# Kernel optimization log

Hardware: AMD Instinct MI355X
Metric: run time of the kernel (lower is better)

## Reference

```python
import jax, jax.numpy as jnp
import numpy as np

DIM = 768
HID = 4 * DIM
NUM_EXPERTS = 8


def setup_inputs() -> dict:
    key = jax.random.key(0)
    ks = jax.random.split(key, 8)
    B, T = 2, 2048
    x = jax.random.normal(ks[0], (B, T, DIM), dtype=jnp.float32)
    mapped_tokens = jax.random.randint(ks[1], (B * T,), 0, NUM_EXPERTS)
    s_in = 1.0 / np.sqrt(DIM)   # nn.Linear init scale for fan_in=DIM
    s_hid = 1.0 / np.sqrt(HID)  # for fan_in=HID
    Wg = jax.random.uniform(ks[2], (NUM_EXPERTS, DIM, HID), jnp.float32, -s_in, s_in)
    bg = jax.random.uniform(ks[3], (NUM_EXPERTS, HID), jnp.float32, -s_in, s_in)
    Wi = jax.random.uniform(ks[4], (NUM_EXPERTS, DIM, HID), jnp.float32, -s_in, s_in)
    bi = jax.random.uniform(ks[5], (NUM_EXPERTS, HID), jnp.float32, -s_in, s_in)
    Wo = jax.random.uniform(ks[6], (NUM_EXPERTS, HID, DIM), jnp.float32, -s_hid, s_hid)
    bo = jax.random.uniform(ks[7], (NUM_EXPERTS, DIM), jnp.float32, -s_hid, s_hid)
    return {"x": x, "mapped_tokens": mapped_tokens, "Wg": Wg, "bg": bg,
            "Wi": Wi, "bi": bi, "Wo": Wo, "bo": bo}


def reference(x, mapped_tokens, Wg, bg, Wi, bi, Wo, bo):
    B, T, C = x.shape
    xf = x.reshape(-1, C)                      # [N, C], N = B*T
    out = jnp.zeros_like(xf)
    E = Wg.shape[0]
    for e in range(E):                         # small fixed expert loop
        h = jax.nn.silu(xf @ Wg[e] + bg[e]) * (xf @ Wi[e] + bi[e])  # [N, 4C]
        y = h @ Wo[e] + bo[e]                  # [N, C]
        out = out + jnp.where((mapped_tokens == e)[:, None], y, 0.0)
    return out.reshape(B, T, C)
```

## Files before the change

kernel.cpp:

```cpp
#include <hip/hip_runtime.h>
#include <hip/hip_bf16.h>
#include <stdint.h>

#define DIM 768
#define HID 3072
#define NE 8
#define NTOK 4096
#define PADROWS 5120
#define MAXT 40

#define M_PO 0
#define M_NTILES 24
#define M_TE 25
#define M_TR 65
#define M_TV 105
#define M_PERM 256
#define XE_OFF (64 * 1024)
#define H_OFF  8126464

typedef short short8 __attribute__((ext_vector_type(8)));
typedef short short4v __attribute__((ext_vector_type(4)));
typedef float f32x4 __attribute__((ext_vector_type(4)));

__device__ __forceinline__ short f2bf(float f) {
  union { float f; uint32_t u; } in; in.f = f;
  uint32_t u = in.u;
  uint32_t r = (u + 0x7fffu + ((u >> 16) & 1u)) >> 16;
  return (short)r;
}

__global__ void route_kernel(const int* __restrict__ map, int* __restrict__ meta) {
  __shared__ int scnt[NE];
  __shared__ int scur[NE];
  int t = threadIdx.x;
  if (t < NE) scnt[t] = 0;
  __syncthreads();
  for (int i = t; i < NTOK; i += 256) atomicAdd(&scnt[map[i]], 1);
  __syncthreads();
  if (t == 0) {
    int acc = 0, nt = 0;
    for (int e = 0; e < NE; ++e) {
      meta[M_PO + e] = acc;
      scur[e] = acc;
      int c = scnt[e];
      for (int r = 0; r < c; r += 128) {
        meta[M_TE + nt] = e;
        meta[M_TR + nt] = acc + r;
        meta[M_TV + nt] = (c - r < 128) ? (c - r) : 128;
        ++nt;
      }
      acc += (c + 127) & ~127;
    }
    meta[M_PO + 8] = acc;
    meta[M_NTILES] = nt;
  }
  for (int i = t; i < PADROWS; i += 256) meta[M_PERM + i] = 0;
  __syncthreads();
  for (int i = t; i < NTOK; i += 256) {
    int e = map[i];
    int slot = atomicAdd(&scur[e], 1);
    meta[M_PERM + slot] = i;
  }
}

__global__ void gather_kernel(const float* __restrict__ x, const int* __restrict__ meta,
                              short* __restrict__ Xe) {
  int id = blockIdx.x * 256 + threadIdx.x;
  if (id >= PADROWS * 96) return;
  int row = id / 96;
  int sub = id - row * 96;
  int tok = meta[M_PERM + row];
  const float* src = x + (size_t)tok * DIM + sub * 8;
  float4 a = *(const float4*)src;
  float4 b = *(const float4*)(src + 4);
  short8 v;
  v[0] = f2bf(a.x); v[1] = f2bf(a.y); v[2] = f2bf(a.z); v[3] = f2bf(a.w);
  v[4] = f2bf(b.x); v[5] = f2bf(b.y); v[6] = f2bf(b.z); v[7] = f2bf(b.w);
  int blk = sub >> 3, s = sub & 7;
  int off = row * (DIM * 2) + blk * 128 + ((s * 16) ^ ((row & 7) << 4));
  *(short8*)((char*)Xe + off) = v;
}

__launch_bounds__(256)
__global__ void gemm1_kernel(const short* __restrict__ Xe, const float* __restrict__ Wg,
                             const float* __restrict__ bg, const float* __restrict__ Wi,
                             const float* __restrict__ bi, const int* __restrict__ meta,
                             short* __restrict__ H) {
  int nt = meta[M_NTILES];
  int ty = blockIdx.y;
  if (ty >= nt) return;
  int e = meta[M_TE + ty], row0 = meta[M_TR + ty], rows = meta[M_TV + ty];
  int j0 = blockIdx.x * 64;
  __shared__ short As[128 * 64];
  __shared__ short Bt[2][64 * 64];
  int tid = threadIdx.x;
  int lane = tid & 63, w = tid >> 6;
  int wm = w >> 1, wn = w & 1;
  const float* W0 = Wg + (size_t)e * DIM * HID;
  const float* W1 = Wi + (size_t)e * DIM * HID;
  f32x4 ag[4][2] = {};
  f32x4 av[4][2] = {};
  int kb = tid >> 4, jb = tid & 15;
  for (int kt = 0; kt < DIM / 64; ++kt) {
    __syncthreads();
    #pragma unroll
    for (int q = 0; q < 4; ++q) {
      int rr = (w * 4 + q) * 8 + (lane >> 3);
      const char* src = (const char*)Xe + (size_t)(row0 + rr) * (DIM * 2) + kt * 128 + (lane & 7) * 16;
      __builtin_amdgcn_global_load_lds((const __attribute__((address_space(1))) void*)src,
                                       (__attribute__((address_space(3))) void*)((char*)As + (w * 4 + q) * 1024),
                                       16, 0, 0);
    }
    #pragma unroll
    for (int mat = 0; mat < 2; ++mat) {
      const float* Wp = (mat == 0) ? W0 : W1;
      const float* base = Wp + (size_t)(kt * 64 + kb * 4) * HID + j0 + jb * 4;
      float4 r0 = *(const float4*)(base);
      float4 r1 = *(const float4*)(base + HID);
      float4 r2 = *(const float4*)(base + 2 * HID);
      float4 r3 = *(const float4*)(base + 3 * HID);
      char* bt = (char*)&Bt[mat][0];
      int col = jb * 4;
      {
        short4v s; s[0]=f2bf(r0.x); s[1]=f2bf(r1.x); s[2]=f2bf(r2.x); s[3]=f2bf(r3.x);
        int c2 = col + 0; *(short4v*)(bt + c2 * 128 + ((kb * 8) ^ ((c2 & 7) << 4))) = s;
      }
      {
        short4v s; s[0]=f2bf(r0.y); s[1]=f2bf(r1.y); s[2]=f2bf(r2.y); s[3]=f2bf(r3.y);
        int c2 = col + 1; *(short4v*)(bt + c2 * 128 + ((kb * 8) ^ ((c2 & 7) << 4))) = s;
      }
      {
        short4v s; s[0]=f2bf(r0.z); s[1]=f2bf(r1.z); s[2]=f2bf(r2.z); s[3]=f2bf(r3.z);
        int c2 = col + 2; *(short4v*)(bt + c2 * 128 + ((kb * 8) ^ ((c2 & 7) << 4))) = s;
      }
      {
        short4v s; s[0]=f2bf(r0.w); s[1]=f2bf(r1.w); s[2]=f2bf(r2.w); s[3]=f2bf(r3.w);
        int c2 = col + 3; *(short4v*)(bt + c2 * 128 + ((kb * 8) ^ ((c2 & 7) << 4))) = s;
      }
    }
    __syncthreads();
    #pragma unroll
    for (int kf = 0; kf < 2; ++kf) {
      short8 af[4];
      #pragma unroll
      for (int m = 0; m < 4; ++m) {
        int r = wm * 64 + m * 16 + (lane & 15);
        int coff = (kf * 64 + (lane >> 4) * 16) ^ ((r & 7) << 4);
        af[m] = *(const short8*)((const char*)As + r * 128 + coff);
      }
      #pragma unroll
      for (int n = 0; n < 2; ++n) {
        int c = wn * 32 + n * 16 + (lane & 15);
        int coff = (kf * 64 + (lane >> 4) * 16) ^ ((c & 7) << 4);
        short8 b0 = *(const short8*)((const char*)&Bt[0][0] + c * 128 + coff);
        short8 b1 = *(const short8*)((const char*)&Bt[1][0] + c * 128 + coff);
        #pragma unroll
        for (int m = 0; m < 4; ++m) {
          ag[m][n] = __builtin_amdgcn_mfma_f32_16x16x32_bf16(af[m], b0, ag[m][n], 0, 0, 0);
          av[m][n] = __builtin_amdgcn_mfma_f32_16x16x32_bf16(af[m], b1, av[m][n], 0, 0, 0);
        }
      }
    }
  }
  #pragma unroll
  for (int n = 0; n < 2; ++n) {
    int c = j0 + wn * 32 + n * 16 + (lane & 15);
    float bgv = bg[e * HID + c];
    float biv = bi[e * HID + c];
    #pragma unroll
    for (int m = 0; m < 4; ++m) {
      #pragma unroll
      for (int r = 0; r < 4; ++r) {
        int rl = wm * 64 + m * 16 + (lane >> 4) * 4 + r;
        if (rl < rows) {
          float g = ag[m][n][r] + bgv;
          float v = av[m][n][r] + biv;
          float h = g / (1.f + __expf(-g)) * v;
          int grow = row0 + rl;
          int off = grow * (HID * 2) + (c >> 6) * 128 + ((2 * (c & 63)) ^ ((grow & 7) << 4));
          *(short*)((char*)H + off) = f2bf(h);
        }
      }
    }
  }
}

__launch_bounds__(256)
__global__ void gemm2_kernel(const short* __restrict__ H, const float* __restrict__ Wo,
                             const float* __restrict__ bo, const int* __restrict__ meta,
                             float* __restrict__ out) {
  int nt = meta[M_NTILES];
  int ty = blockIdx.y;
  if (ty >= nt) return;
  int e = meta[M_TE + ty], row0 = meta[M_TR + ty], rows = meta[M_TV + ty];
  int j0 = blockIdx.x * 64;
  __shared__ short As[128 * 64];
  __shared__ short Bt[64 * 64];
  int tid = threadIdx.x;
  int lane = tid & 63, w = tid >> 6;
  int wm = w >> 1, wn = w & 1;
  const float* W2 = Wo + (size_t)e * HID * DIM;
  f32x4 acc[4][2] = {};
  int kb = tid >> 4, jb = tid & 15;
  for (int kt = 0; kt < HID / 64; ++kt) {
    __syncthreads();
    #pragma unroll
    for (int q = 0; q < 4; ++q) {
      int rr = (w * 4 + q) * 8 + (lane >> 3);
      const char* src = (const char*)H + (size_t)(row0 + rr) * (HID * 2) + kt * 128 + (lane & 7) * 16;
      __builtin_amdgcn_global_load_lds((const __attribute__((address_space(1))) void*)src,
                                       (__attribute__((address_space(3))) void*)((char*)As + (w * 4 + q) * 1024),
                                       16, 0, 0);
    }
    {
      const float* base = W2 + (size_t)(kt * 64 + kb * 4) * DIM + j0 + jb * 4;
      float4 r0 = *(const float4*)(base);
      float4 r1 = *(const float4*)(base + DIM);
      float4 r2 = *(const float4*)(base + 2 * DIM);
      float4 r3 = *(const float4*)(base + 3 * DIM);
      char* bt = (char*)&Bt[0];
      int col = jb * 4;
      {
        short4v s; s[0]=f2bf(r0.x); s[1]=f2bf(r1.x); s[2]=f2bf(r2.x); s[3]=f2bf(r3.x);
        int c2 = col + 0; *(short4v*)(bt + c2 * 128 + ((kb * 8) ^ ((c2 & 7) << 4))) = s;
      }
      {
        short4v s; s[0]=f2bf(r0.y); s[1]=f2bf(r1.y); s[2]=f2bf(r2.y); s[3]=f2bf(r3.y);
        int c2 = col + 1; *(short4v*)(bt + c2 * 128 + ((kb * 8) ^ ((c2 & 7) << 4))) = s;
      }
      {
        short4v s; s[0]=f2bf(r0.z); s[1]=f2bf(r1.z); s[2]=f2bf(r2.z); s[3]=f2bf(r3.z);
        int c2 = col + 2; *(short4v*)(bt + c2 * 128 + ((kb * 8) ^ ((c2 & 7) << 4))) = s;
      }
      {
        short4v s; s[0]=f2bf(r0.w); s[1]=f2bf(r1.w); s[2]=f2bf(r2.w); s[3]=f2bf(r3.w);
        int c2 = col + 3; *(short4v*)(bt + c2 * 128 + ((kb * 8) ^ ((c2 & 7) << 4))) = s;
      }
    }
    __syncthreads();
    #pragma unroll
    for (int kf = 0; kf < 2; ++kf) {
      short8 af[4];
      #pragma unroll
      for (int m = 0; m < 4; ++m) {
        int r = wm * 64 + m * 16 + (lane & 15);
        int coff = (kf * 64 + (lane >> 4) * 16) ^ ((r & 7) << 4);
        af[m] = *(const short8*)((const char*)As + r * 128 + coff);
      }
      #pragma unroll
      for (int n = 0; n < 2; ++n) {
        int c = wn * 32 + n * 16 + (lane & 15);
        int coff = (kf * 64 + (lane >> 4) * 16) ^ ((c & 7) << 4);
        short8 b0 = *(const short8*)((const char*)&Bt[0] + c * 128 + coff);
        #pragma unroll
        for (int m = 0; m < 4; ++m) {
          acc[m][n] = __builtin_amdgcn_mfma_f32_16x16x32_bf16(af[m], b0, acc[m][n], 0, 0, 0);
        }
      }
    }
  }
  #pragma unroll
  for (int n = 0; n < 2; ++n) {
    int c = j0 + wn * 32 + n * 16 + (lane & 15);
    float bov = bo[e * DIM + c];
    #pragma unroll
    for (int m = 0; m < 4; ++m) {
      #pragma unroll
      for (int r = 0; r < 4; ++r) {
        int rl = wm * 64 + m * 16 + (lane >> 4) * 4 + r;
        if (rl < rows) {
          int tok = meta[M_PERM + row0 + rl];
          out[(size_t)tok * DIM + c] = acc[m][n][r] + bov;
        }
      }
    }
  }
}

extern "C" void kernel_launch(void* const* d_in, const int* in_sizes, int n_in,
                              void* d_out, int out_size, void* d_ws, size_t ws_size,
                              hipStream_t stream) {
  (void)in_sizes; (void)n_in; (void)out_size; (void)ws_size;
  const float* x   = (const float*)d_in[0];
  const int*   map = (const int*)d_in[1];
  const float* Wg  = (const float*)d_in[2];
  const float* bg  = (const float*)d_in[3];
  const float* Wi  = (const float*)d_in[4];
  const float* bi  = (const float*)d_in[5];
  const float* Wo  = (const float*)d_in[6];
  const float* bo  = (const float*)d_in[7];
  float* out = (float*)d_out;
  int* meta = (int*)d_ws;
  short* Xe = (short*)((char*)d_ws + XE_OFF);
  short* H  = (short*)((char*)d_ws + H_OFF);

  hipLaunchKernelGGL(route_kernel, dim3(1), dim3(256), 0, stream, map, meta);
  hipLaunchKernelGGL(gather_kernel, dim3(PADROWS * 96 / 256), dim3(256), 0, stream, x, meta, Xe);
  hipLaunchKernelGGL(gemm1_kernel, dim3(HID / 64, MAXT), dim3(256), 0, stream,
                     Xe, Wg, bg, Wi, bi, meta, H);
  hipLaunchKernelGGL(gemm2_kernel, dim3(DIM / 64, MAXT), dim3(256), 0, stream,
                     H, Wo, bo, meta, out);
}
```

Measured before the change: 412.0 us.

## Software-pipeline both expert GEMMs with double-buffered A tiles and register-prefetched weights

Both GEMM kernels now prefetch the next K-tile: activations go asynchronously into a second LDS buffer, and fp32 weights are loaded into registers while the current tile's MFMAs run. The bf16 weight tile is written to LDS after a barrier, so global latency overlaps with compute instead of stalling each iteration. The thread-to-(kb,jb) mapping is swapped, bf16 conversion uses the library intrinsic, and launch bounds request 3 blocks per CU. The costs are more registers and double the A-tile LDS, and the single-buffered B tile still needs two barriers per iteration.

```diff
diff --git a/kernel.cpp b/kernel.cpp
--- a/kernel.cpp
+++ b/kernel.cpp
@@ -22,11 +22,9 @@
 typedef short short4v __attribute__((ext_vector_type(4)));
 typedef float f32x4 __attribute__((ext_vector_type(4)));
 
-__device__ __forceinline__ short f2bf(float f) {
-  union { float f; uint32_t u; } in; in.f = f;
-  uint32_t u = in.u;
-  uint32_t r = (u + 0x7fffu + ((u >> 16) & 1u)) >> 16;
-  return (short)r;
+__device__ __forceinline__ short bfs(float f) {
+  __hip_bfloat16 h = __float2bfloat16(f);
+  short s; __builtin_memcpy(&s, &h, 2); return s;
 }
 
 __global__ void route_kernel(const int* __restrict__ map, int* __restrict__ meta) {
@@ -74,14 +72,45 @@
   float4 a = *(const float4*)src;
   float4 b = *(const float4*)(src + 4);
   short8 v;
-  v[0] = f2bf(a.x); v[1] = f2bf(a.y); v[2] = f2bf(a.z); v[3] = f2bf(a.w);
-  v[4] = f2bf(b.x); v[5] = f2bf(b.y); v[6] = f2bf(b.z); v[7] = f2bf(b.w);
+  v[0] = bfs(a.x); v[1] = bfs(a.y); v[2] = bfs(a.z); v[3] = bfs(a.w);
+  v[4] = bfs(b.x); v[5] = bfs(b.y); v[6] = bfs(b.z); v[7] = bfs(b.w);
   int blk = sub >> 3, s = sub & 7;
   int off = row * (DIM * 2) + blk * 128 + ((s * 16) ^ ((row & 7) << 4));
   *(short8*)((char*)Xe + off) = v;
 }
 
-__launch_bounds__(256)
+__device__ __forceinline__ void write_bt2(char* bt0, char* bt1,
+                                          const float4 (&br)[2][4], int kb, int jb) {
+  char* bts[2] = {bt0, bt1};
+  #pragma unroll
+  for (int mat = 0; mat < 2; ++mat) {
+    #pragma unroll
+    for (int i = 0; i < 4; ++i) {
+      int c2 = jb * 4 + i;
+      short4v s;
+      s[0] = bfs(((const float*)&br[mat][0])[i]);
+      s[1] = bfs(((const float*)&br[mat][1])[i]);
+      s[2] = bfs(((const float*)&br[mat][2])[i]);
+      s[3] = bfs(((const float*)&br[mat][3])[i]);
+      *(short4v*)(bts[mat] + c2 * 128 + ((kb * 8) ^ ((c2 & 7) << 4))) = s;
+    }
+  }
+}
+
+__device__ __forceinline__ void write_bt1(char* bt, const float4 (&br)[4], int kb, int jb) {
+  #pragma unroll
+  for (int i = 0; i < 4; ++i) {
+    int c2 = jb * 4 + i;
+    short4v s;
+    s[0] = bfs(((const float*)&br[0])[i]);
+    s[1] = bfs(((const float*)&br[1])[i]);
+    s[2] = bfs(((const float*)&br[2])[i]);
+    s[3] = bfs(((const float*)&br[3])[i]);
+    *(short4v*)(bt + c2 * 128 + ((kb * 8) ^ ((c2 & 7) << 4))) = s;
+  }
+}
+
+__launch_bounds__(256, 3)
 __global__ void gemm1_kernel(const short* __restrict__ Xe, const float* __restrict__ Wg,
                              const float* __restrict__ bg, const float* __restrict__ Wi,
                              const float* __restrict__ bi, const int* __restrict__ meta,
@@ -91,54 +120,53 @@
   if (ty >= nt) return;
   int e = meta[M_TE + ty], row0 = meta[M_TR + ty], rows = meta[M_TV + ty];
   int j0 = blockIdx.x * 64;
-  __shared__ short As[128 * 64];
+  __shared__ short As[2][128 * 64];
   __shared__ short Bt[2][64 * 64];
   int tid = threadIdx.x;
   int lane = tid & 63, w = tid >> 6;
   int wm = w >> 1, wn = w & 1;
+  int kb = tid & 15, jb = tid >> 4;
   const float* W0 = Wg + (size_t)e * DIM * HID;
   const float* W1 = Wi + (size_t)e * DIM * HID;
   f32x4 ag[4][2] = {};
   f32x4 av[4][2] = {};
-  int kb = tid >> 4, jb = tid & 15;
-  for (int kt = 0; kt < DIM / 64; ++kt) {
-    __syncthreads();
-    #pragma unroll
-    for (int q = 0; q < 4; ++q) {
-      int rr = (w * 4 + q) * 8 + (lane >> 3);
-      const char* src = (const char*)Xe + (size_t)(row0 + rr) * (DIM * 2) + kt * 128 + (lane & 7) * 16;
-      __builtin_amdgcn_global_load_lds((const __attribute__((address_space(1))) void*)src,
-                                       (__attribute__((address_space(3))) void*)((char*)As + (w * 4 + q) * 1024),
-                                       16, 0, 0);
-    }
-    #pragma unroll
-    for (int mat = 0; mat < 2; ++mat) {
-      const float* Wp = (mat == 0) ? W0 : W1;
-      const float* base = Wp + (size_t)(kt * 64 + kb * 4) * HID + j0 + jb * 4;
-      float4 r0 = *(const float4*)(base);
-      float4 r1 = *(const float4*)(base + HID);
-      float4 r2 = *(const float4*)(base + 2 * HID);
-      float4 r3 = *(const float4*)(base + 3 * HID);
-      char* bt = (char*)&Bt[mat][0];
-      int col = jb * 4;
-      {
-        short4v s; s[0]=f2bf(r0.x); s[1]=f2bf(r1.x); s[2]=f2bf(r2.x); s[3]=f2bf(r3.x);
-        int c2 = col + 0; *(short4v*)(bt + c2 * 128 + ((kb * 8) ^ ((c2 & 7) << 4))) = s;
-      }
-      {
-        short4v s; s[0]=f2bf(r0.y); s[1]=f2bf(r1.y); s[2]=f2bf(r2.y); s[3]=f2bf(r3.y);
-        int c2 = col + 1; *(short4v*)(bt + c2 * 128 + ((kb * 8) ^ ((c2 & 7) << 4))) = s;
-      }
-      {
-        short4v s; s[0]=f2bf(r0.z); s[1]=f2bf(r1.z); s[2]=f2bf(r2.z); s[3]=f2bf(r3.z);
-        int c2 = col + 2; *(short4v*)(bt + c2 * 128 + ((kb * 8) ^ ((c2 & 7) << 4))) = s;
-      }
-      {
-        short4v s; s[0]=f2bf(r0.w); s[1]=f2bf(r1.w); s[2]=f2bf(r2.w); s[3]=f2bf(r3.w);
-        int c2 = col + 3; *(short4v*)(bt + c2 * 128 + ((kb * 8) ^ ((c2 & 7) << 4))) = s;
-      }
-    }
-    __syncthreads();
+  float4 br[2][4];
+
+  #pragma unroll
+  for (int mat = 0; mat < 2; ++mat) {
+    const float* base = (mat ? W1 : W0) + (size_t)(kb * 4) * HID + j0 + jb * 4;
+    #pragma unroll
+    for (int r = 0; r < 4; ++r) br[mat][r] = *(const float4*)(base + r * HID);
+  }
+  #pragma unroll
+  for (int q = 0; q < 4; ++q) {
+    const char* src = (const char*)Xe + (size_t)(row0 + (w * 4 + q) * 8 + (lane >> 3)) * (DIM * 2)
+                      + (lane & 7) * 16;
+    __builtin_amdgcn_global_load_lds((const __attribute__((address_space(1))) void*)src,
+                                     (__attribute__((address_space(3))) void*)((char*)&As[0][0] + (w * 4 + q) * 1024),
+                                     16, 0, 0);
+  }
+  write_bt2((char*)&Bt[0][0], (char*)&Bt[1][0], br, kb, jb);
+  __syncthreads();
+
+  int cur = 0;
+  for (int kt = 0; kt < 12; ++kt) {
+    if (kt < 11) {
+      #pragma unroll
+      for (int mat = 0; mat < 2; ++mat) {
+        const float* base = (mat ? W1 : W0) + (size_t)((kt + 1) * 64 + kb * 4) * HID + j0 + jb * 4;
+        #pragma unroll
+        for (int r = 0; r < 4; ++r) br[mat][r] = *(const float4*)(base + r * HID);
+      }
+      #pragma unroll
+      for (int q = 0; q < 4; ++q) {
+        const char* src = (const char*)Xe + (size_t)(row0 + (w * 4 + q) * 8 + (lane >> 3)) * (DIM * 2)
+                          + (kt + 1) * 128 + (lane & 7) * 16;
+        __builtin_amdgcn_global_load_lds((const __attribute__((address_space(1))) void*)src,
+                                         (__attribute__((address_space(3))) void*)((char*)&As[cur ^ 1][0] + (w * 4 + q) * 1024),
+                                         16, 0, 0);
+      }
+    }
     #pragma unroll
     for (int kf = 0; kf < 2; ++kf) {
       short8 af[4];
@@ -146,7 +174,7 @@
       for (int m = 0; m < 4; ++m) {
         int r = wm * 64 + m * 16 + (lane & 15);
         int coff = (kf * 64 + (lane >> 4) * 16) ^ ((r & 7) << 4);
-        af[m] = *(const short8*)((const char*)As + r * 128 + coff);
+        af[m] = *(const short8*)((const char*)&As[cur][0] + r * 128 + coff);
       }
       #pragma unroll
       for (int n = 0; n < 2; ++n) {
@@ -161,7 +189,12 @@
         }
       }
     }
-  }
+    asm volatile("s_waitcnt lgkmcnt(0)\n\ts_barrier" ::: "memory");
+    if (kt < 11) write_bt2((char*)&Bt[0][0], (char*)&Bt[1][0], br, kb, jb);
+    __syncthreads();
+    cur ^= 1;
+  }
+
   #pragma unroll
   for (int n = 0; n < 2; ++n) {
     int c = j0 + wn * 32 + n * 16 + (lane & 15);
@@ -178,14 +211,14 @@
           float h = g / (1.f + __expf(-g)) * v;
           int grow = row0 + rl;
           int off = grow * (HID * 2) + (c >> 6) * 128 + ((2 * (c & 63)) ^ ((grow & 7) << 4));
-          *(short*)((char*)H + off) = f2bf(h);
+          *(short*)((char*)H + off) = bfs(h);
         }
       }
     }
   }
 }
 
-__launch_bounds__(256)
+__launch_bounds__(256, 3)
 __global__ void gemm2_kernel(const short* __restrict__ H, const float* __restrict__ Wo,
                              const float* __restrict__ bo, const int* __restrict__ meta,
                              float* __restrict__ out) {
@@ -194,50 +227,45 @@
   if (ty >= nt) return;
   int e = meta[M_TE + ty], row0 = meta[M_TR + ty], rows = meta[M_TV + ty];
   int j0 = blockIdx.x * 64;
-  __shared__ short As[128 * 64];
+  __shared__ short As[2][128 * 64];
   __shared__ short Bt[64 * 64];
   int tid = threadIdx.x;
   int lane = tid & 63, w = tid >> 6;
   int wm = w >> 1, wn = w & 1;
+  int kb = tid & 15, jb = tid >> 4;
   const float* W2 = Wo + (size_t)e * HID * DIM;
   f32x4 acc[4][2] = {};
-  int kb = tid >> 4, jb = tid & 15;
-  for (int kt = 0; kt < HID / 64; ++kt) {
-    __syncthreads();
-    #pragma unroll
-    for (int q = 0; q < 4; ++q) {
-      int rr = (w * 4 + q) * 8 + (lane >> 3);
-      const char* src = (const char*)H + (size_t)(row0 + rr) * (HID * 2) + kt * 128 + (lane & 7) * 16;
-      __builtin_amdgcn_global_load_lds((const __attribute__((address_space(1))) void*)src,
-                                       (__attribute__((address_space(3))) void*)((char*)As + (w * 4 + q) * 1024),
-                                       16, 0, 0);
-    }
-    {
-      const float* base = W2 + (size_t)(kt * 64 + kb * 4) * DIM + j0 + jb * 4;
-      float4 r0 = *(const float4*)(base);
-      float4 r1 = *(const float4*)(base + DIM);
-      float4 r2 = *(const float4*)(base + 2 * DIM);
-      float4 r3 = *(const float4*)(base + 3 * DIM);
-      char* bt = (char*)&Bt[0];
-      int col = jb * 4;
-      {
-        short4v s; s[0]=f2bf(r0.x); s[1]=f2bf(r1.x); s[2]=f2bf(r2.x); s[3]=f2bf(r3.x);
-        int c2 = col + 0; *(short4v*)(bt + c2 * 128 + ((kb * 8) ^ ((c2 & 7) << 4))) = s;
-      }
-      {
-        short4v s; s[0]=f2bf(r0.y); s[1]=f2bf(r1.y); s[2]=f2bf(r2.y); s[3]=f2bf(r3.y);
-        int c2 = col + 1; *(short4v*)(bt + c2 * 128 + ((kb * 8) ^ ((c2 & 7) << 4))) = s;
-      }
-      {
-        short4v s; s[0]=f2bf(r0.z); s[1]=f2bf(r1.z); s[2]=f2bf(r2.z); s[3]=f2bf(r3.z);
-        int c2 = col + 2; *(short4v*)(bt + c2 * 128 + ((kb * 8) ^ ((c2 & 7) << 4))) = s;
-      }
-      {
-        short4v s; s[0]=f2bf(r0.w); s[1]=f2bf(r1.w); s[2]=f2bf(r2.w); s[3]=f2bf(r3.w);
-        int c2 = col + 3; *(short4v*)(bt + c2 * 128 + ((kb * 8) ^ ((c2 & 7) << 4))) = s;
-      }
-    }
-    __syncthreads();
+  float4 br[4];
+
+  #pragma unroll
+  for (int r = 0; r < 4; ++r)
+    br[r] = *(const float4*)(W2 + (size_t)(kb * 4 + r) * DIM + j0 + jb * 4);
+  #pragma unroll
+  for (int q = 0; q < 4; ++q) {
+    const char* src = (const char*)H + (size_t)(row0 + (w * 4 + q) * 8 + (lane >> 3)) * (HID * 2)
+                      + (lane & 7) * 16;
+    __builtin_amdgcn_global_load_lds((const __attribute__((address_space(1))) void*)src,
+                                     (__attribute__((address_space(3))) void*)((char*)&As[0][0] + (w * 4 + q) * 1024),
+                                     16, 0, 0);
+  }
+  write_bt1((char*)&Bt[0], br, kb, jb);
+  __syncthreads();
+
+  int cur = 0;
+  for (int kt = 0; kt < 48; ++kt) {
+    if (kt < 47) {
+      #pragma unroll
+      for (int r = 0; r < 4; ++r)
+        br[r] = *(const float4*)(W2 + (size_t)((kt + 1) * 64 + kb * 4 + r) * DIM + j0 + jb * 4);
+      #pragma unroll
+      for (int q = 0; q < 4; ++q) {
+        const char* src = (const char*)H + (size_t)(row0 + (w * 4 + q) * 8 + (lane >> 3)) * (HID * 2)
+                          + (kt + 1) * 128 + (lane & 7) * 16;
+        __builtin_amdgcn_global_load_lds((const __attribute__((address_space(1))) void*)src,
+                                         (__attribute__((address_space(3))) void*)((char*)&As[cur ^ 1][0] + (w * 4 + q) * 1024),
+                                         16, 0, 0);
+      }
+    }
     #pragma unroll
     for (int kf = 0; kf < 2; ++kf) {
       short8 af[4];
@@ -245,7 +273,7 @@
       for (int m = 0; m < 4; ++m) {
         int r = wm * 64 + m * 16 + (lane & 15);
         int coff = (kf * 64 + (lane >> 4) * 16) ^ ((r & 7) << 4);
-        af[m] = *(const short8*)((const char*)As + r * 128 + coff);
+        af[m] = *(const short8*)((const char*)&As[cur][0] + r * 128 + coff);
       }
       #pragma unroll
       for (int n = 0; n < 2; ++n) {
@@ -258,7 +286,12 @@
         }
       }
     }
-  }
+    asm volatile("s_waitcnt lgkmcnt(0)\n\ts_barrier" ::: "memory");
+    if (kt < 47) write_bt1((char*)&Bt[0], br, kb, jb);
+    __syncthreads();
+    cur ^= 1;
+  }
+
   #pragma unroll
   for (int n = 0; n < 2; ++n) {
     int c = j0 + wn * 32 + n * 16 + (lane & 15);
```

New measurement: 419.4 us. About the same (+1.8%).
